# Optimization experiments

Measured on AMD Instinct MI355X. Metric: run time of the kernel, lower is better.

## Reference

```python
import jax, jax.numpy as jnp
import numpy as np
import math

NUM_HEADS = 32
NUM_KV_HEADS = 8
HEAD_DIM = 128
HIDDEN = 4096
BATCH = 2
SEQ = 2048
MASK_MIN = -1e9


def _rope(x, cos, sin):
    # x: [B, S, H, D], cos/sin: [S, D/2]
    d2 = x.shape[-1] // 2
    x1, x2 = x[..., :d2], x[..., d2:]
    c = cos[None, :, None, :]
    s = sin[None, :, None, :]
    return jnp.concatenate([x1 * c - x2 * s, x2 * c + x1 * s], axis=-1)


def setup_inputs() -> dict:
    key = jax.random.key(0)
    k1, k2, k3 = jax.random.split(key, 3)
    hidden_states = jax.random.normal(k1, (BATCH, SEQ, HIDDEN), dtype=jnp.float32) * 0.02
    Wqkv = jax.random.normal(k2, (HIDDEN, (NUM_HEADS + 2 * NUM_KV_HEADS) * HEAD_DIM), dtype=jnp.float32) * (HIDDEN ** -0.5)
    Wo = jax.random.normal(k3, (NUM_HEADS * HEAD_DIM, HIDDEN), dtype=jnp.float32) * (HIDDEN ** -0.5)
    pos = np.arange(SEQ, dtype=np.float32)
    inv_freq = 1.0 / (10000.0 ** (np.arange(0, HEAD_DIM, 2, dtype=np.float32) / HEAD_DIM))
    freqs = np.outer(pos, inv_freq)  # [S, D/2]
    cos = jnp.asarray(np.cos(freqs), dtype=jnp.float32)
    sin = jnp.asarray(np.sin(freqs), dtype=jnp.float32)
    # causal additive mask [B, 1, S, S]
    causal = np.triu(np.full((SEQ, SEQ), MASK_MIN, dtype=np.float32), k=1)
    attention_mask = jnp.broadcast_to(jnp.asarray(causal)[None, None], (BATCH, 1, SEQ, SEQ))
    return {"hidden_states": hidden_states, "Wqkv": Wqkv, "Wo": Wo,
            "cos": cos, "sin": sin, "attention_mask": attention_mask}


def reference(hidden_states, Wqkv, Wo, cos, sin, attention_mask):
    B, S, H = hidden_states.shape
    n_rep = NUM_HEADS // NUM_KV_HEADS
    qkv = jnp.einsum('bsh,hd->bsd', hidden_states, Wqkv)
    q_end = NUM_HEADS * HEAD_DIM
    k_end = q_end + NUM_KV_HEADS * HEAD_DIM
    q = qkv[..., :q_end].reshape(B, S, NUM_HEADS, HEAD_DIM)
    k = qkv[..., q_end:k_end].reshape(B, S, NUM_KV_HEADS, HEAD_DIM)
    v = qkv[..., k_end:].reshape(B, S, NUM_KV_HEADS, HEAD_DIM)
    q = _rope(q, cos, sin)
    k = _rope(k, cos, sin)
    # repeat_kv: expand kv heads to query heads
    k = jnp.repeat(k, n_rep, axis=2)  # [B, S, NH, D]
    v = jnp.repeat(v, n_rep, axis=2)
    scores = jnp.einsum('bqhd,bkhd->bhqk', q, k) / math.sqrt(HEAD_DIM)
    scores = scores + attention_mask
    scores = jnp.maximum(scores, jnp.finfo(scores.dtype).min)
    probs = jax.nn.softmax(scores.astype(jnp.float32), axis=-1).astype(q.dtype)
    attn = jnp.einsum('bhqk,bkhd->bqhd', probs, v)  # [B, S, NH, D]
    attn = attn.reshape(B, S, NUM_HEADS * HEAD_DIM)
    return jnp.einsum('bsd,dh->bsh', attn, Wo)
```

## Files before the change

kernel.cpp:

```cpp
#include <hip/hip_runtime.h>

typedef unsigned short u16;
typedef __bf16 bf16x8 __attribute__((ext_vector_type(8)));
typedef float f32x4 __attribute__((ext_vector_type(4)));
typedef float f32x16 __attribute__((ext_vector_type(16)));
typedef u16 u16x4 __attribute__((ext_vector_type(4)));

#define SEQ 2048
#define NQKV 6144
#define HID 4096

__device__ inline u16 f2bf(float f) {
  union { float f; unsigned u; } x; x.f = f;
  unsigned r = x.u + 0x7fffu + ((x.u >> 16) & 1u);
  return (u16)(r >> 16);
}
__device__ inline float bf2f(u16 u) {
  union { unsigned u; float f; } x; x.u = ((unsigned)u) << 16;
  return x.f;
}
__device__ inline f32x16 mfma32(bf16x8 a, bf16x8 b, f32x16 c) {
  return __builtin_amdgcn_mfma_f32_32x32x16_bf16(a, b, c, 0, 0, 0);
}
__device__ inline unsigned cvtpk(float lo, float hi) {
  unsigned r;
  asm("v_cvt_pk_bf16_f32 %0, %1, %2" : "=v"(r) : "v"(lo), "v"(hi));
  return r;
}
__device__ inline void gload16(const void* g, void* l) {
  __builtin_amdgcn_global_load_lds((const __attribute__((address_space(1))) void*)g,
                                   (__attribute__((address_space(3))) void*)l,
                                   16, 0, 0);
}


__global__ __launch_bounds__(256) void conv_kernel(const float* __restrict__ in,
                                                   u16* __restrict__ out) {
  int i = (blockIdx.x * 256 + threadIdx.x) * 4;
  int m = i >> 12, k = i & 4095;
  float4 v = *(const float4*)(in + i);
  u16x4 o;
  o[0] = f2bf(v.x); o[1] = f2bf(v.y); o[2] = f2bf(v.z); o[3] = f2bf(v.w);
  int p = m >> 8, r = m & 255;
  int t = k >> 5, kc = (k >> 3) & 3, e = k & 7;
  int slot = ((r >> 5) << 7) + (kc << 5) + (r & 31);
  *(u16x4*)(out + ((size_t)(p * 128 + t) * 1024 + slot) * 8 + e) = o;
}

__global__ __launch_bounds__(256) void transconv_qkv_kernel(const float* __restrict__ in,
                                                            u16* __restrict__ out) {
  __shared__ u16 tile[32][33];
  int c0 = blockIdx.x * 32, r0 = blockIdx.y * 32;
  int tx = threadIdx.x & 31, ty = threadIdx.x >> 5;
  for (int i = 0; i < 4; ++i)
    tile[ty + 8 * i][tx] = f2bf(in[(size_t)(r0 + ty + 8 * i) * NQKV + c0 + tx]);
  __syncthreads();
  int t = r0 >> 5;
  for (int i = 0; i < 4; ++i) {
    int n = c0 + ty + 8 * i;
    int p = n / 384, pc = n - p * 384;
    int kc = tx >> 3, e = tx & 7;
    int slot = ((pc >> 5) << 7) + (kc << 5) + (pc & 31);
    out[((size_t)(p * 128 + t) * 1536 + slot) * 8 + e] = tile[tx][ty + 8 * i];
  }
}

__global__ __launch_bounds__(256) void transconv_wo_kernel(const float* __restrict__ in,
                                                           u16* __restrict__ out) {
  __shared__ u16 tile[32][33];
  int c0 = blockIdx.x * 32, r0 = blockIdx.y * 32;
  int tx = threadIdx.x & 31, ty = threadIdx.x >> 5;
  for (int i = 0; i < 4; ++i)
    tile[ty + 8 * i][tx] = f2bf(in[(size_t)(r0 + ty + 8 * i) * HID + c0 + tx]);
  __syncthreads();
  int t = r0 >> 5;
  for (int i = 0; i < 4; ++i) {
    int n = c0 + ty + 8 * i;
    int p = n >> 8, pc = n & 255;
    int kc = tx >> 3, e = tx & 7;
    int slot = ((pc >> 5) << 7) + (kc << 5) + (pc & 31);
    out[((size_t)(p * 128 + t) * 1024 + slot) * 8 + e] = tile[tx][ty + 8 * i];
  }
}

__global__ __launch_bounds__(512, 2) void gemm32_kernel(const u16* __restrict__ At,
                                                        const u16* __restrict__ Btl,
                                                        u16* __restrict__ C,
                                                        int M, int N, int K, int nby) {
  __shared__ __align__(16) u16 As[3][256 * 32];
  __shared__ __align__(16) u16 Bs[3][384 * 32];
  int nwg = gridDim.x;
  int bid = blockIdx.x;
  int s = (bid & 7) * (nwg >> 3) + (bid >> 3);
  int by = s % nby, bx = s / nby;
  int row0 = by * 256, col0 = bx * 384;
  int tid = threadIdx.x, w = tid >> 6, l = tid & 63;
  int wm = w >> 2, wn = w & 3;
  int l31 = l & 31, lh = l >> 5;
  const u16* Ap = At + (size_t)by * 128 * 1024 * 8;
  const u16* Bp = Btl + (size_t)bx * 128 * 1536 * 8;
  int nkt = K >> 5;

  f32x16 acc[4][3] = {};

#define STA32(tt, bf)                                                         \
  { _Pragma("unroll")                                                         \
    for (int j = 0; j < 2; ++j) {                                             \
      int cid = j * 512 + tid;                                                \
      gload16(Ap + ((size_t)(tt) * 1024 + cid) * 8, &As[bf][cid * 8]);        \
    } }
#define STB32(tt, bf)                                                         \
  { _Pragma("unroll")                                                         \
    for (int j = 0; j < 3; ++j) {                                             \
      int cid = j * 512 + tid;                                                \
      gload16(Bp + ((size_t)(tt) * 1536 + cid) * 8, &Bs[bf][cid * 8]);        \
    } }
#define RA32(bf, im, ks, dst)                                                 \
  { int slot = ((wm * 4 + (im)) << 7) + (((ks) * 2 + lh) << 5) + l31;         \
    dst = *(const bf16x8*)&As[bf][slot * 8]; }
#define RB32(bf, in, ks, dst)                                                 \
  { int slot = ((wn * 3 + (in)) << 7) + (((ks) * 2 + lh) << 5) + l31;         \
    dst = *(const bf16x8*)&Bs[bf][slot * 8]; }

  STA32(0, 0); STB32(0, 0); STA32(1, 1); STB32(1, 1);
  asm volatile("s_waitcnt vmcnt(5)" ::: "memory");
  __builtin_amdgcn_s_barrier();

  int cur = 0;
  for (int t = 0; t < nkt; ++t) {
    int nb = cur + 2; if (nb >= 3) nb -= 3;
    bool pf = (t + 2 < nkt);
    bf16x8 a0, a1, a2, a3, b0, b1, b2;
    RA32(cur, 0, 0, a0); RA32(cur, 1, 0, a1); RA32(cur, 2, 0, a2); RA32(cur, 3, 0, a3);
    RB32(cur, 0, 0, b0); RB32(cur, 1, 0, b1); RB32(cur, 2, 0, b2);
    if (pf) STA32(t + 2, nb);
    __builtin_amdgcn_s_setprio(1);
    acc[0][0] = mfma32(a0, b0, acc[0][0]); acc[0][1] = mfma32(a0, b1, acc[0][1]);
    acc[0][2] = mfma32(a0, b2, acc[0][2]);
    acc[1][0] = mfma32(a1, b0, acc[1][0]); acc[1][1] = mfma32(a1, b1, acc[1][1]);
    acc[1][2] = mfma32(a1, b2, acc[1][2]);
    acc[2][0] = mfma32(a2, b0, acc[2][0]); acc[2][1] = mfma32(a2, b1, acc[2][1]);
    acc[2][2] = mfma32(a2, b2, acc[2][2]);
    acc[3][0] = mfma32(a3, b0, acc[3][0]); acc[3][1] = mfma32(a3, b1, acc[3][1]);
    acc[3][2] = mfma32(a3, b2, acc[3][2]);
    __builtin_amdgcn_s_setprio(0);
    RA32(cur, 0, 1, a0); RA32(cur, 1, 1, a1); RA32(cur, 2, 1, a2); RA32(cur, 3, 1, a3);
    RB32(cur, 0, 1, b0); RB32(cur, 1, 1, b1); RB32(cur, 2, 1, b2);
    if (pf) STB32(t + 2, nb);
    __builtin_amdgcn_s_setprio(1);
    acc[0][0] = mfma32(a0, b0, acc[0][0]); acc[0][1] = mfma32(a0, b1, acc[0][1]);
    acc[0][2] = mfma32(a0, b2, acc[0][2]);
    acc[1][0] = mfma32(a1, b0, acc[1][0]); acc[1][1] = mfma32(a1, b1, acc[1][1]);
    acc[1][2] = mfma32(a1, b2, acc[1][2]);
    acc[2][0] = mfma32(a2, b0, acc[2][0]); acc[2][1] = mfma32(a2, b1, acc[2][1]);
    acc[2][2] = mfma32(a2, b2, acc[2][2]);
    acc[3][0] = mfma32(a3, b0, acc[3][0]); acc[3][1] = mfma32(a3, b1, acc[3][1]);
    acc[3][2] = mfma32(a3, b2, acc[3][2]);
    __builtin_amdgcn_s_setprio(0);
    if (pf)               { asm volatile("s_waitcnt vmcnt(5)" ::: "memory"); }
    else if (t + 1 < nkt) { asm volatile("s_waitcnt vmcnt(0)" ::: "memory"); }
    __builtin_amdgcn_s_barrier();
    cur = cur + 1 == 3 ? 0 : cur + 1;
  }
#undef STA32
#undef STB32
#undef RA32
#undef RB32

#pragma unroll
  for (int im = 0; im < 4; ++im)
#pragma unroll
    for (int in = 0; in < 3; ++in)
#pragma unroll
      for (int reg = 0; reg < 16; ++reg) {
        int row = row0 + wm * 128 + im * 32 + (reg & 3) + 8 * (reg >> 2) + 4 * lh;
        int col = col0 + wn * 96 + in * 32 + l31;
        C[(size_t)row * N + col] = f2bf(acc[im][in][reg]);
      }
}

__global__ __launch_bounds__(512, 2) void gemm32_o_kernel(const u16* __restrict__ At,
                                                          const u16* __restrict__ Btl,
                                                          float* __restrict__ C,
                                                          int M, int N, int K, int nby) {
  __shared__ __align__(16) u16 As[3][256 * 32];
  __shared__ __align__(16) u16 Bs[3][256 * 32];
  int nwg = gridDim.x;
  int bid = blockIdx.x;
  int s = (bid & 7) * (nwg >> 3) + (bid >> 3);
  int by = s % nby, bx = s / nby;
  int row0 = by * 256, col0 = bx * 256;
  int tid = threadIdx.x, w = tid >> 6, l = tid & 63;
  int wm = w >> 2, wn = w & 3;
  int l31 = l & 31, lh = l >> 5;
  const u16* Ap = At + (size_t)by * 128 * 1024 * 8;
  const u16* Bp = Btl + (size_t)bx * 128 * 1024 * 8;
  int nkt = K >> 5;

  f32x16 acc[4][2] = {};

#define STAO(tt, bf)                                                          \
  { _Pragma("unroll")                                                         \
    for (int j = 0; j < 2; ++j) {                                             \
      int cid = j * 512 + tid;                                                \
      gload16(Ap + ((size_t)(tt) * 1024 + cid) * 8, &As[bf][cid * 8]);        \
    } }
#define STBO(tt, bf)                                                          \
  { _Pragma("unroll")                                                         \
    for (int j = 0; j < 2; ++j) {                                             \
      int cid = j * 512 + tid;                                                \
      gload16(Bp + ((size_t)(tt) * 1024 + cid) * 8, &Bs[bf][cid * 8]);        \
    } }
#define RAO(bf, im, ks, dst)                                                  \
  { int slot = ((wm * 4 + (im)) << 7) + (((ks) * 2 + lh) << 5) + l31;         \
    dst = *(const bf16x8*)&As[bf][slot * 8]; }
#define RBO(bf, in, ks, dst)                                                  \
  { int slot = ((wn * 2 + (in)) << 7) + (((ks) * 2 + lh) << 5) + l31;         \
    dst = *(const bf16x8*)&Bs[bf][slot * 8]; }

  STAO(0, 0); STBO(0, 0); STAO(1, 1); STBO(1, 1);
  asm volatile("s_waitcnt vmcnt(4)" ::: "memory");
  __builtin_amdgcn_s_barrier();

  int cur = 0;
  for (int t = 0; t < nkt; ++t) {
    int nb = cur + 2; if (nb >= 3) nb -= 3;
    bool pf = (t + 2 < nkt);
    bf16x8 a0, a1, a2, a3, b0, b1;
    RAO(cur, 0, 0, a0); RAO(cur, 1, 0, a1); RAO(cur, 2, 0, a2); RAO(cur, 3, 0, a3);
    RBO(cur, 0, 0, b0); RBO(cur, 1, 0, b1);
    if (pf) STAO(t + 2, nb);
    __builtin_amdgcn_s_setprio(1);
    acc[0][0] = mfma32(a0, b0, acc[0][0]); acc[0][1] = mfma32(a0, b1, acc[0][1]);
    acc[1][0] = mfma32(a1, b0, acc[1][0]); acc[1][1] = mfma32(a1, b1, acc[1][1]);
    acc[2][0] = mfma32(a2, b0, acc[2][0]); acc[2][1] = mfma32(a2, b1, acc[2][1]);
    acc[3][0] = mfma32(a3, b0, acc[3][0]); acc[3][1] = mfma32(a3, b1, acc[3][1]);
    __builtin_amdgcn_s_setprio(0);
    RAO(cur, 0, 1, a0); RAO(cur, 1, 1, a1); RAO(cur, 2, 1, a2); RAO(cur, 3, 1, a3);
    RBO(cur, 0, 1, b0); RBO(cur, 1, 1, b1);
    if (pf) STBO(t + 2, nb);
    __builtin_amdgcn_s_setprio(1);
    acc[0][0] = mfma32(a0, b0, acc[0][0]); acc[0][1] = mfma32(a0, b1, acc[0][1]);
    acc[1][0] = mfma32(a1, b0, acc[1][0]); acc[1][1] = mfma32(a1, b1, acc[1][1]);
    acc[2][0] = mfma32(a2, b0, acc[2][0]); acc[2][1] = mfma32(a2, b1, acc[2][1]);
    acc[3][0] = mfma32(a3, b0, acc[3][0]); acc[3][1] = mfma32(a3, b1, acc[3][1]);
    __builtin_amdgcn_s_setprio(0);
    if (pf)               { asm volatile("s_waitcnt vmcnt(4)" ::: "memory"); }
    else if (t + 1 < nkt) { asm volatile("s_waitcnt vmcnt(0)" ::: "memory"); }
    __builtin_amdgcn_s_barrier();
    cur = cur + 1 == 3 ? 0 : cur + 1;
  }
#undef STAO
#undef STBO
#undef RAO
#undef RBO

#pragma unroll
  for (int im = 0; im < 4; ++im)
#pragma unroll
    for (int in = 0; in < 2; ++in)
#pragma unroll
      for (int reg = 0; reg < 16; ++reg) {
        int row = row0 + wm * 128 + im * 32 + (reg & 3) + 8 * (reg >> 2) + 4 * lh;
        int col = col0 + wn * 64 + in * 32 + l31;
        C[(size_t)row * N + col] = acc[im][in][reg];
      }
}

__global__ __launch_bounds__(256) void rope_kernel(u16* __restrict__ qkv,
                                                   const float* __restrict__ cosb,
                                                   const float* __restrict__ sinb) {
  int idx = blockIdx.x * 256 + threadIdx.x;
  int d = (idx & 15) * 4;
  int head = (idx >> 4) % 40;
  int m = idx / (16 * 40);
  int s = m & (SEQ - 1);
  int col = head < 32 ? head * 128 : 4096 + (head - 32) * 128;
  u16* p = qkv + (size_t)m * NQKV + col;
  u16x4 x1 = *(u16x4*)(p + d);
  u16x4 x2 = *(u16x4*)(p + d + 64);
  float4 cv = *(const float4*)(cosb + s * 64 + d);
  float4 sv = *(const float4*)(sinb + s * 64 + d);
  float cc[4] = {cv.x, cv.y, cv.z, cv.w};
  float ss[4] = {sv.x, sv.y, sv.z, sv.w};
  u16x4 o1, o2;
#pragma unroll
  for (int j = 0; j < 4; ++j) {
    float a = bf2f(x1[j]), b = bf2f(x2[j]);
    o1[j] = f2bf(a * cc[j] - b * ss[j]);
    o2[j] = f2bf(b * cc[j] + a * ss[j]);
  }
  *(u16x4*)(p + d) = o1;
  *(u16x4*)(p + d + 64) = o2;
}

__global__ __launch_bounds__(256) void vtrans_kernel(const u16* __restrict__ qkv,
                                                     u16* __restrict__ Vt) {
  __shared__ u16 tile[32][33];
  int bid = blockIdx.x;
  int dt = bid & 3;
  int st = (bid >> 2) & 63;
  int bk = bid >> 8;
  int b = bk >> 3, kvh = bk & 7;
  int tx = threadIdx.x & 31, ty = threadIdx.x >> 5;
  for (int i = 0; i < 4; ++i) {
    int s = st * 32 + ty + 8 * i;
    tile[ty + 8 * i][tx] = qkv[(size_t)(b * SEQ + s) * NQKV + 5120 + kvh * 128 + dt * 32 + tx];
  }
  __syncthreads();
  for (int i = 0; i < 4; ++i) {
    int d = dt * 32 + ty + 8 * i;
    Vt[((size_t)bk * 128 + d) * SEQ + st * 32 + tx] = tile[tx][ty + 8 * i];
  }
}

__global__ __launch_bounds__(256, 2) void flash_kernel(const u16* __restrict__ qkv,
                                                       const u16* __restrict__ Vt,
                                                       u16* __restrict__ attnT) {
  const float C2 = 0.12751740f;
  int bid = blockIdx.x;
  int bh = bid & 63;
  int pr = bid >> 6;
  int h = bh & 31;
  int b = bh >> 5;
  int w = threadIdx.x >> 6, l = threadIdx.x & 63;
  int hv = l >> 5;
  int q32 = l & 31;
  int kvh = h >> 2;

  __shared__ __align__(16) u16 Ks[2][64 * 128];
  __shared__ __align__(16) u16 Vs[2][128 * 64];

  const u16* kb = qkv + (size_t)(b * SEQ) * NQKV + 4096 + kvh * 128;
  const u16* vtb = Vt + (size_t)(b * 8 + kvh) * 128 * SEQ;

#define STAGEKV(TT, BF)                                                       \
  { _Pragma("unroll")                                                         \
    for (int i = 0; i < 4; ++i) {                                             \
      int ck = w * 4 + i;                                                     \
      int rk = ck * 4 + (l >> 4);                                             \
      gload16(kb + (size_t)((TT) * 64 + rk) * NQKV + (((l & 15) ^ (rk & 7)) * 8), \
              &Ks[BF][ck * 512]);                                             \
      int rv = ck * 8 + (l >> 3);                                             \
      gload16(vtb + (size_t)rv * SEQ + (TT) * 64 + (((l & 7) ^ (rv & 7)) * 8), \
              &Vs[BF][ck * 512]);                                             \
    } }

  for (int pass = 0; pass < 2; ++pass) {
    int qc = pass ? 15 - pr : pr;
    int q0 = qc * 128 + w * 32;
    int qg = q0 + q32;
    __syncthreads();

    bf16x8 qf[8];
    {
      const u16* qr = qkv + (size_t)(b * SEQ + qg) * NQKV + h * 128 + hv * 8;
#pragma unroll
      for (int d0 = 0; d0 < 8; ++d0) qf[d0] = *(const bf16x8*)(qr + d0 * 16);
    }
    f32x16 o[4] = {};
    float mreg = -1e30f, lreg = 0.f;
    int ktend = 2 * qc + 1;
    int mykt = 2 * qc + (w >> 1);

    STAGEKV(0, 0);
    for (int kt = 0; kt <= ktend; ++kt) {
      int buf = kt & 1;
      if (kt < ktend) {
        STAGEKV(kt + 1, buf ^ 1);
        asm volatile("s_waitcnt vmcnt(8)" ::: "memory");
      } else {
        asm volatile("s_waitcnt vmcnt(0)" ::: "memory");
      }
      __builtin_amdgcn_s_barrier();

      if (kt <= mykt) {
        f32x16 s0 = {}, s1 = {};
        int swzk = q32 & 7;
#pragma unroll
        for (int d0 = 0; d0 < 8; ++d0) {
          int sl = (((d0 * 2 + hv) ^ swzk) * 8);
          bf16x8 k0 = *(const bf16x8*)&Ks[buf][q32 * 128 + sl];
          bf16x8 k1 = *(const bf16x8*)&Ks[buf][(32 + q32) * 128 + sl];
          s0 = mfma32(k0, qf[d0], s0);
          s1 = mfma32(k1, qf[d0], s1);
        }
        if (kt == mykt) {
#pragma unroll
          for (int r = 0; r < 16; ++r) {
            int kloc = (r & 3) + 8 * (r >> 2) + 4 * hv;
            if (kt * 64 + kloc > qg) s0[r] = -1e30f;
            if (kt * 64 + 32 + kloc > qg) s1[r] = -1e30f;
          }
        }
        float pm = -1e30f;
#pragma unroll
        for (int r = 0; r < 16; ++r) {
          pm = fmaxf(pm, s0[r]);
          pm = fmaxf(pm, s1[r]);
        }
        pm = fmaxf(pm, __shfl_xor(pm, 32));
        if (!__all(pm - mreg <= 62.746f)) {
          float mnew = fmaxf(mreg, pm);
          float al = exp2f((mreg - mnew) * C2);
          lreg *= al;
#pragma unroll
          for (int r = 0; r < 16; ++r) {
            o[0][r] *= al; o[1][r] *= al; o[2][r] *= al; o[3][r] *= al;
          }
          mreg = mnew;
        }
        float rs = 0.f;
#pragma unroll
        for (int r = 0; r < 16; ++r) {
          s0[r] = exp2f((s0[r] - mreg) * C2); rs += s0[r];
          s1[r] = exp2f((s1[r] - mreg) * C2); rs += s1[r];
        }
        rs += __shfl_xor(rs, 32);
        lreg += rs;
        bf16x8 pa[4];
#define MKPA(KSI, SP, RB)                                                     \
        { unsigned wA = cvtpk(SP[(RB) + 0], SP[(RB) + 1]);                    \
          unsigned wB = cvtpk(SP[(RB) + 2], SP[(RB) + 3]);                    \
          unsigned wC = cvtpk(SP[(RB) + 4], SP[(RB) + 5]);                    \
          unsigned wD = cvtpk(SP[(RB) + 6], SP[(RB) + 7]);                    \
          unsigned sA = __shfl_xor(wA, 32), sB = __shfl_xor(wB, 32);          \
          unsigned sC = __shfl_xor(wC, 32), sD = __shfl_xor(wD, 32);          \
          union { unsigned u[4]; bf16x8 v; } pk;                              \
          pk.u[0] = hv ? sC : wA; pk.u[1] = hv ? sD : wB;                     \
          pk.u[2] = hv ? wC : sA; pk.u[3] = hv ? wD : sB;                     \
          pa[KSI] = pk.v; }
        MKPA(0, s0, 0) MKPA(1, s0, 8) MKPA(2, s1, 0) MKPA(3, s1, 8)
#undef MKPA
#pragma unroll
        for (int db = 0; db < 4; ++db) {
          int rv = db * 32 + q32;
          int swz = rv & 7;
#pragma unroll
          for (int ks = 0; ks < 4; ++ks) {
            bf16x8 vf = *(const bf16x8*)&Vs[buf][rv * 64 + (((ks * 2 + hv) ^ swz) * 8)];
            o[db] = mfma32(vf, pa[ks], o[db]);
          }
        }
      }
    }
    float invl = 1.0f / lreg;
    {
      int m = b * SEQ + qg;
      int p = m >> 8, r = m & 255;
      u16* op = attnT + ((size_t)(p * 128 + h * 4) * 1024 +
                         ((r >> 5) << 7) + (r & 31)) * 8 + 4 * hv;
#pragma unroll
      for (int db = 0; db < 4; ++db)
#pragma unroll
        for (int g = 0; g < 4; ++g) {
          unsigned w0 = cvtpk(o[db][g * 4 + 0] * invl, o[db][g * 4 + 1] * invl);
          unsigned w1 = cvtpk(o[db][g * 4 + 2] * invl, o[db][g * 4 + 3] * invl);
          uint2 val; val.x = w0; val.y = w1;
          *(uint2*)(op + db * 8192 + g * 256) = val;
        }
    }
  }
#undef STAGEKV
}

extern "C" void kernel_launch(void* const* d_in, const int* in_sizes, int n_in,
                              void* d_out, int out_size, void* d_ws, size_t ws_size,
                              hipStream_t stream) {
  const float* hidden = (const float*)d_in[0];
  const float* Wqkv = (const float*)d_in[1];
  const float* Wo = (const float*)d_in[2];
  const float* cosb = (const float*)d_in[3];
  const float* sinb = (const float*)d_in[4];
  float* out = (float*)d_out;

  char* ws = (char*)d_ws;
  u16* R1 = (u16*)ws;
  u16* R2 = (u16*)(ws + 50331648);
  u16* R3 = (u16*)(ws + 100663296);

  conv_kernel<<<16384, 256, 0, stream>>>(hidden, R3);
  transconv_qkv_kernel<<<dim3(6144 / 32, 4096 / 32), 256, 0, stream>>>(Wqkv, R1);
  gemm32_kernel<<<256, 512, 0, stream>>>(R3, R1, R2, 4096, 6144, 4096, 16);
  rope_kernel<<<10240, 256, 0, stream>>>(R2, cosb, sinb);
  vtrans_kernel<<<4096, 256, 0, stream>>>(R2, R3);
  flash_kernel<<<512, 256, 0, stream>>>(R2, R3, R1);
  transconv_wo_kernel<<<dim3(4096 / 32, 4096 / 32), 256, 0, stream>>>(Wo, R2);
  gemm32_o_kernel<<<256, 512, 0, stream>>>(R1, R2, out, 4096, 4096, 4096, 16);
}
```

Before: 509.7 us.

## Use 16 waves per block in both GEMMs, halving per-wave M tile

```diff
diff --git a/kernel.cpp b/kernel.cpp
--- a/kernel.cpp
+++ b/kernel.cpp
@@ -83,10 +83,10 @@
   }
 }
 
-__global__ __launch_bounds__(512, 2) void gemm32_kernel(const u16* __restrict__ At,
-                                                        const u16* __restrict__ Btl,
-                                                        u16* __restrict__ C,
-                                                        int M, int N, int K, int nby) {
+__global__ __launch_bounds__(1024) void gemm32_kernel(const u16* __restrict__ At,
+                                                      const u16* __restrict__ Btl,
+                                                      u16* __restrict__ C,
+                                                      int M, int N, int K, int nby) {
   __shared__ __align__(16) u16 As[3][256 * 32];
   __shared__ __align__(16) u16 Bs[3][384 * 32];
   int nwg = gridDim.x;
@@ -101,37 +101,33 @@
   const u16* Bp = Btl + (size_t)bx * 128 * 1536 * 8;
   int nkt = K >> 5;
 
-  f32x16 acc[4][3] = {};
+  f32x16 acc[2][3] = {};
 
 #define STA32(tt, bf)                                                         \
-  { _Pragma("unroll")                                                         \
-    for (int j = 0; j < 2; ++j) {                                             \
-      int cid = j * 512 + tid;                                                \
-      gload16(Ap + ((size_t)(tt) * 1024 + cid) * 8, &As[bf][cid * 8]);        \
-    } }
+  gload16(Ap + ((size_t)(tt) * 1024 + tid) * 8, &As[bf][tid * 8]);
 #define STB32(tt, bf)                                                         \
-  { _Pragma("unroll")                                                         \
-    for (int j = 0; j < 3; ++j) {                                             \
-      int cid = j * 512 + tid;                                                \
-      gload16(Bp + ((size_t)(tt) * 1536 + cid) * 8, &Bs[bf][cid * 8]);        \
-    } }
+  { gload16(Bp + ((size_t)(tt) * 1536 + tid) * 8, &Bs[bf][tid * 8]);          \
+    if (tid < 512)                                                            \
+      gload16(Bp + ((size_t)(tt) * 1536 + 1024 + tid) * 8,                    \
+              &Bs[bf][(1024 + tid) * 8]); }
 #define RA32(bf, im, ks, dst)                                                 \
-  { int slot = ((wm * 4 + (im)) << 7) + (((ks) * 2 + lh) << 5) + l31;         \
+  { int slot = ((wm * 2 + (im)) << 7) + (((ks) * 2 + lh) << 5) + l31;         \
     dst = *(const bf16x8*)&As[bf][slot * 8]; }
 #define RB32(bf, in, ks, dst)                                                 \
   { int slot = ((wn * 3 + (in)) << 7) + (((ks) * 2 + lh) << 5) + l31;         \
     dst = *(const bf16x8*)&Bs[bf][slot * 8]; }
 
   STA32(0, 0); STB32(0, 0); STA32(1, 1); STB32(1, 1);
-  asm volatile("s_waitcnt vmcnt(5)" ::: "memory");
+  if (w < 8) { asm volatile("s_waitcnt vmcnt(3)" ::: "memory"); }
+  else       { asm volatile("s_waitcnt vmcnt(2)" ::: "memory"); }
   __builtin_amdgcn_s_barrier();
 
   int cur = 0;
   for (int t = 0; t < nkt; ++t) {
     int nb = cur + 2; if (nb >= 3) nb -= 3;
     bool pf = (t + 2 < nkt);
-    bf16x8 a0, a1, a2, a3, b0, b1, b2;
-    RA32(cur, 0, 0, a0); RA32(cur, 1, 0, a1); RA32(cur, 2, 0, a2); RA32(cur, 3, 0, a3);
+    bf16x8 a0, a1, b0, b1, b2;
+    RA32(cur, 0, 0, a0); RA32(cur, 1, 0, a1);
     RB32(cur, 0, 0, b0); RB32(cur, 1, 0, b1); RB32(cur, 2, 0, b2);
     if (pf) STA32(t + 2, nb);
     __builtin_amdgcn_s_setprio(1);
@@ -139,12 +135,8 @@
     acc[0][2] = mfma32(a0, b2, acc[0][2]);
     acc[1][0] = mfma32(a1, b0, acc[1][0]); acc[1][1] = mfma32(a1, b1, acc[1][1]);
     acc[1][2] = mfma32(a1, b2, acc[1][2]);
-    acc[2][0] = mfma32(a2, b0, acc[2][0]); acc[2][1] = mfma32(a2, b1, acc[2][1]);
-    acc[2][2] = mfma32(a2, b2, acc[2][2]);
-    acc[3][0] = mfma32(a3, b0, acc[3][0]); acc[3][1] = mfma32(a3, b1, acc[3][1]);
-    acc[3][2] = mfma32(a3, b2, acc[3][2]);
     __builtin_amdgcn_s_setprio(0);
-    RA32(cur, 0, 1, a0); RA32(cur, 1, 1, a1); RA32(cur, 2, 1, a2); RA32(cur, 3, 1, a3);
+    RA32(cur, 0, 1, a0); RA32(cur, 1, 1, a1);
     RB32(cur, 0, 1, b0); RB32(cur, 1, 1, b1); RB32(cur, 2, 1, b2);
     if (pf) STB32(t + 2, nb);
     __builtin_amdgcn_s_setprio(1);
@@ -152,13 +144,13 @@
     acc[0][2] = mfma32(a0, b2, acc[0][2]);
     acc[1][0] = mfma32(a1, b0, acc[1][0]); acc[1][1] = mfma32(a1, b1, acc[1][1]);
     acc[1][2] = mfma32(a1, b2, acc[1][2]);
-    acc[2][0] = mfma32(a2, b0, acc[2][0]); acc[2][1] = mfma32(a2, b1, acc[2][1]);
-    acc[2][2] = mfma32(a2, b2, acc[2][2]);
-    acc[3][0] = mfma32(a3, b0, acc[3][0]); acc[3][1] = mfma32(a3, b1, acc[3][1]);
-    acc[3][2] = mfma32(a3, b2, acc[3][2]);
     __builtin_amdgcn_s_setprio(0);
-    if (pf)               { asm volatile("s_waitcnt vmcnt(5)" ::: "memory"); }
-    else if (t + 1 < nkt) { asm volatile("s_waitcnt vmcnt(0)" ::: "memory"); }
+    if (pf) {
+      if (w < 8) { asm volatile("s_waitcnt vmcnt(3)" ::: "memory"); }
+      else       { asm volatile("s_waitcnt vmcnt(2)" ::: "memory"); }
+    } else if (t + 1 < nkt) {
+      asm volatile("s_waitcnt vmcnt(0)" ::: "memory");
+    }
     __builtin_amdgcn_s_barrier();
     cur = cur + 1 == 3 ? 0 : cur + 1;
   }
@@ -168,21 +160,21 @@
 #undef RB32
 
 #pragma unroll
-  for (int im = 0; im < 4; ++im)
+  for (int im = 0; im < 2; ++im)
 #pragma unroll
     for (int in = 0; in < 3; ++in)
 #pragma unroll
       for (int reg = 0; reg < 16; ++reg) {
-        int row = row0 + wm * 128 + im * 32 + (reg & 3) + 8 * (reg >> 2) + 4 * lh;
+        int row = row0 + wm * 64 + im * 32 + (reg & 3) + 8 * (reg >> 2) + 4 * lh;
         int col = col0 + wn * 96 + in * 32 + l31;
         C[(size_t)row * N + col] = f2bf(acc[im][in][reg]);
       }
 }
 
-__global__ __launch_bounds__(512, 2) void gemm32_o_kernel(const u16* __restrict__ At,
-                                                          const u16* __restrict__ Btl,
-                                                          float* __restrict__ C,
-                                                          int M, int N, int K, int nby) {
+__global__ __launch_bounds__(1024) void gemm32_o_kernel(const u16* __restrict__ At,
+                                                        const u16* __restrict__ Btl,
+                                                        float* __restrict__ C,
+                                                        int M, int N, int K, int nby) {
   __shared__ __align__(16) u16 As[3][256 * 32];
   __shared__ __align__(16) u16 Bs[3][256 * 32];
   int nwg = gridDim.x;
@@ -197,55 +189,43 @@
   const u16* Bp = Btl + (size_t)bx * 128 * 1024 * 8;
   int nkt = K >> 5;
 
-  f32x16 acc[4][2] = {};
+  f32x16 acc[2][2] = {};
 
 #define STAO(tt, bf)                                                          \
-  { _Pragma("unroll")                                                         \
-    for (int j = 0; j < 2; ++j) {                                             \
-      int cid = j * 512 + tid;                                                \
-      gload16(Ap + ((size_t)(tt) * 1024 + cid) * 8, &As[bf][cid * 8]);        \
-    } }
+  gload16(Ap + ((size_t)(tt) * 1024 + tid) * 8, &As[bf][tid * 8]);
 #define STBO(tt, bf)                                                          \
-  { _Pragma("unroll")                                                         \
-    for (int j = 0; j < 2; ++j) {                                             \
-      int cid = j * 512 + tid;                                                \
-      gload16(Bp + ((size_t)(tt) * 1024 + cid) * 8, &Bs[bf][cid * 8]);        \
-    } }
+  gload16(Bp + ((size_t)(tt) * 1024 + tid) * 8, &Bs[bf][tid * 8]);
 #define RAO(bf, im, ks, dst)                                                  \
-  { int slot = ((wm * 4 + (im)) << 7) + (((ks) * 2 + lh) << 5) + l31;         \
+  { int slot = ((wm * 2 + (im)) << 7) + (((ks) * 2 + lh) << 5) + l31;         \
     dst = *(const bf16x8*)&As[bf][slot * 8]; }
 #define RBO(bf, in, ks, dst)                                                  \
   { int slot = ((wn * 2 + (in)) << 7) + (((ks) * 2 + lh) << 5) + l31;         \
     dst = *(const bf16x8*)&Bs[bf][slot * 8]; }
 
   STAO(0, 0); STBO(0, 0); STAO(1, 1); STBO(1, 1);
-  asm volatile("s_waitcnt vmcnt(4)" ::: "memory");
+  asm volatile("s_waitcnt vmcnt(2)" ::: "memory");
   __builtin_amdgcn_s_barrier();
 
   int cur = 0;
   for (int t = 0; t < nkt; ++t) {
     int nb = cur + 2; if (nb >= 3) nb -= 3;
     bool pf = (t + 2 < nkt);
-    bf16x8 a0, a1, a2, a3, b0, b1;
-    RAO(cur, 0, 0, a0); RAO(cur, 1, 0, a1); RAO(cur, 2, 0, a2); RAO(cur, 3, 0, a3);
+    bf16x8 a0, a1, b0, b1;
+    RAO(cur, 0, 0, a0); RAO(cur, 1, 0, a1);
     RBO(cur, 0, 0, b0); RBO(cur, 1, 0, b1);
     if (pf) STAO(t + 2, nb);
     __builtin_amdgcn_s_setprio(1);
     acc[0][0] = mfma32(a0, b0, acc[0][0]); acc[0][1] = mfma32(a0, b1, acc[0][1]);
     acc[1][0] = mfma32(a1, b0, acc[1][0]); acc[1][1] = mfma32(a1, b1, acc[1][1]);
-    acc[2][0] = mfma32(a2, b0, acc[2][0]); acc[2][1] = mfma32(a2, b1, acc[2][1]);
-    acc[3][0] = mfma32(a3, b0, acc[3][0]); acc[3][1] = mfma32(a3, b1, acc[3][1]);
     __builtin_amdgcn_s_setprio(0);
-    RAO(cur, 0, 1, a0); RAO(cur, 1, 1, a1); RAO(cur, 2, 1, a2); RAO(cur, 3, 1, a3);
+    RAO(cur, 0, 1, a0); RAO(cur, 1, 1, a1);
     RBO(cur, 0, 1, b0); RBO(cur, 1, 1, b1);
     if (pf) STBO(t + 2, nb);
     __builtin_amdgcn_s_setprio(1);
     acc[0][0] = mfma32(a0, b0, acc[0][0]); acc[0][1] = mfma32(a0, b1, acc[0][1]);
     acc[1][0] = mfma32(a1, b0, acc[1][0]); acc[1][1] = mfma32(a1, b1, acc[1][1]);
-    acc[2][0] = mfma32(a2, b0, acc[2][0]); acc[2][1] = mfma32(a2, b1, acc[2][1]);
-    acc[3][0] = mfma32(a3, b0, acc[3][0]); acc[3][1] = mfma32(a3, b1, acc[3][1]);
     __builtin_amdgcn_s_setprio(0);
-    if (pf)               { asm volatile("s_waitcnt vmcnt(4)" ::: "memory"); }
+    if (pf)               { asm volatile("s_waitcnt vmcnt(2)" ::: "memory"); }
     else if (t + 1 < nkt) { asm volatile("s_waitcnt vmcnt(0)" ::: "memory"); }
     __builtin_amdgcn_s_barrier();
     cur = cur + 1 == 3 ? 0 : cur + 1;
@@ -256,12 +236,12 @@
 #undef RBO
 
 #pragma unroll
-  for (int im = 0; im < 4; ++im)
+  for (int im = 0; im < 2; ++im)
 #pragma unroll
     for (int in = 0; in < 2; ++in)
 #pragma unroll
       for (int reg = 0; reg < 16; ++reg) {
-        int row = row0 + wm * 128 + im * 32 + (reg & 3) + 8 * (reg >> 2) + 4 * lh;
+        int row = row0 + wm * 64 + im * 32 + (reg & 3) + 8 * (reg >> 2) + 4 * lh;
         int col = col0 + wn * 64 + in * 32 + l31;
         C[(size_t)row * N + col] = acc[im][in][reg];
       }
@@ -481,10 +461,10 @@
 
   conv_kernel<<<16384, 256, 0, stream>>>(hidden, R3);
   transconv_qkv_kernel<<<dim3(6144 / 32, 4096 / 32), 256, 0, stream>>>(Wqkv, R1);
-  gemm32_kernel<<<256, 512, 0, stream>>>(R3, R1, R2, 4096, 6144, 4096, 16);
+  gemm32_kernel<<<256, 1024, 0, stream>>>(R3, R1, R2, 4096, 6144, 4096, 16);
   rope_kernel<<<10240, 256, 0, stream>>>(R2, cosb, sinb);
   vtrans_kernel<<<4096, 256, 0, stream>>>(R2, R3);
   flash_kernel<<<512, 256, 0, stream>>>(R2, R3, R1);
   transconv_wo_kernel<<<dim3(4096 / 32, 4096 / 32), 256, 0, stream>>>(Wo, R2);
-  gemm32_o_kernel<<<256, 512, 0, stream>>>(R1, R2, out, 4096, 4096, 4096, 16);
-}
+  gemm32_o_kernel<<<256, 1024, 0, stream>>>(R1, R2, out, 4096, 4096, 4096, 16);
+}
```

Result: slower. 582.6 us (+14.3%).
